# Kernel optimization log

Hardware: AMD Instinct MI355X
Metric: run time of the kernel (lower is better)

The kernel has to match this reference:

```python
import jax, jax.numpy as jnp
import numpy as np

B, T, D_IN, H, OUT = 512, 512, 64, 256, 64
EPS = 1e-5


def _ln(x, w, b):
    m = x.mean(-1, keepdims=True)
    v = ((x - m) ** 2).mean(-1, keepdims=True)
    return (x - m) / jnp.sqrt(v + EPS) * w + b


def _cell(x, h_prev, Wg, bg, gnw, gnb, Wc, bc, cnw, cnb):
    # LayerNormGRU cell
    combined = jnp.concatenate([x, h_prev], axis=-1)          # [B, D+H]
    rz = _ln(combined @ Wg.T + bg, gnw, gnb)                  # [B, 2H]
    r, z = jnp.split(rz, 2, axis=-1)
    r, z = jax.nn.sigmoid(r), jax.nn.sigmoid(z)
    combined_r = jnp.concatenate([x, r * h_prev], axis=-1)
    n = jnp.tanh(_ln(combined_r @ Wc.T + bc, cnw, cnb))       # [B, H]
    return (1.0 - z) * h_prev + z * n


def setup_inputs() -> dict:
    key = jax.random.key(0)
    ks = jax.random.split(key, 24)

    def uni(k, shape, fan_in):
        lim = 1.0 / np.sqrt(fan_in)
        return jax.random.uniform(k, shape, jnp.float32, -lim, lim)

    d0 = D_IN + H   # layer 0 cell input width
    d1 = H + H      # layer 1 cell input width
    return {
        "x": jax.random.normal(ks[0], (B, T, D_IN), jnp.float32),
        # layer 0
        "Wg0": uni(ks[1], (2 * H, d0), d0), "bg0": uni(ks[2], (2 * H,), d0),
        "gnw0": jnp.ones((2 * H,), jnp.float32), "gnb0": jnp.zeros((2 * H,), jnp.float32),
        "Wc0": uni(ks[3], (H, d0), d0), "bc0": uni(ks[4], (H,), d0),
        "cnw0": jnp.ones((H,), jnp.float32), "cnb0": jnp.zeros((H,), jnp.float32),
        # layer 1
        "Wg1": uni(ks[5], (2 * H, d1), d1), "bg1": uni(ks[6], (2 * H,), d1),
        "gnw1": jnp.ones((2 * H,), jnp.float32), "gnb1": jnp.zeros((2 * H,), jnp.float32),
        "Wc1": uni(ks[7], (H, d1), d1), "bc1": uni(ks[8], (H,), d1),
        "cnw1": jnp.ones((H,), jnp.float32), "cnb1": jnp.zeros((H,), jnp.float32),
        # output head
        "fcW": uni(ks[9], (OUT, H), H), "fcb": uni(ks[10], (OUT,), H),
    }


def reference(x, Wg0, bg0, gnw0, gnb0, Wc0, bc0, cnw0, cnb0,
              Wg1, bg1, gnw1, gnb1, Wc1, bc1, cnw1, cnb1, fcW, fcb):
    b = x.shape[0]
    h_init = (jnp.zeros((b, H), x.dtype), jnp.zeros((b, H), x.dtype))

    def step(carry, xt):
        h0, h1 = carry
        h0 = _cell(xt, h0, Wg0, bg0, gnw0, gnb0, Wc0, bc0, cnw0, cnb0)
        h1 = _cell(h0, h1, Wg1, bg1, gnw1, gnb1, Wc1, bc1, cnw1, cnb1)
        return (h0, h1), None

    (h0, h1), _ = jax.lax.scan(step, h_init, jnp.swapaxes(x, 0, 1))  # scan over T
    return h1 @ fcW.T + fcb  # [B, OUT]
```

## Files before the change

kernel.cpp:

```cpp
#include <hip/hip_runtime.h>


#define B_   512
#define T_   512
#define DIN  64
#define H_   256
#define OUT_ 64
#define EPS_ 1e-5f

typedef __attribute__((ext_vector_type(8))) short bf16x8;
typedef __attribute__((ext_vector_type(4))) float f32x4;

__device__ __forceinline__ unsigned short f2bf(float f) {
  unsigned int u = __float_as_uint(f);
  u += 0x7fffu + ((u >> 16) & 1u);
  return (unsigned short)(u >> 16);
}
__device__ __forceinline__ float bfh(unsigned short u) {
  return __uint_as_float(((unsigned int)u) << 16);
}
__device__ __forceinline__ float sigm_(float x) {
  return __builtin_amdgcn_rcpf(1.f + __expf(-x));
}
__device__ __forceinline__ float tanh_(float x) {
  return 1.f - 2.f * __builtin_amdgcn_rcpf(__expf(2.f * x) + 1.f);
}
template<int C>
__device__ __forceinline__ float dpp_add(float v) {
  int r = __builtin_amdgcn_update_dpp(0, __float_as_int(v), C, 0xF, 0xF, false);
  return v + __int_as_float(r);
}
__device__ __forceinline__ float red16(float v) {
  v = dpp_add<0x121>(v);
  v = dpp_add<0x122>(v);
  v = dpp_add<0x124>(v);
  v = dpp_add<0x128>(v);
  return v;
}

#define PIN8A(a) asm volatile("" : "+a"(a[0]), "+a"(a[1]), "+a"(a[2]), "+a"(a[3]), \
                                   "+a"(a[4]), "+a"(a[5]), "+a"(a[6]), "+a"(a[7]))

__global__ void prep_frag(const float* __restrict__ w, unsigned short* __restrict__ dst,
                          int N, int Ksrc, int koff) {
  int gid = blockIdx.x * 256 + threadIdx.x;
  if (gid >= N * 256) return;
  int n = gid >> 8, k = gid & 255;
  int idx = (((n >> 4) * 8 + (k >> 5)) * 64 + ((n & 15) + 16 * ((k >> 3) & 3))) * 8 + (k & 7);
  dst[idx] = f2bf(w[(size_t)n * Ksrc + koff + k]);
}

__global__ void prep_wx(const float* __restrict__ wg, const float* __restrict__ wc,
                        unsigned short* __restrict__ dst, int KX, int Kg, int Kc) {
  int gid = blockIdx.x * 256 + threadIdx.x;
  if (gid >= 768 * KX) return;
  int n = gid / KX, k = gid - n * KX;
  float v = (n < 512) ? wg[(size_t)n * Kg + k] : wc[(size_t)(n - 512) * Kc + k];
  dst[gid] = f2bf(v);
}

__global__ void bias_cat(const float* __restrict__ bg, const float* __restrict__ bc,
                         float* __restrict__ dst) {
  int i = blockIdx.x * 256 + threadIdx.x;
  if (i < 768) dst[i] = (i < 512) ? bg[i] : bc[i - 512];
}

__device__ __forceinline__ void precomp_tile(
    const void* __restrict__ Asrc, const unsigned short* __restrict__ wx,
    const float* __restrict__ bias, unsigned short* __restrict__ Pc,
    int TC, int t0, int KX, int AFP32,
    int mi, int nb, unsigned short* A_s, unsigned short* B_s, int t256)
{
  const int lane = t256 & 63, wv = t256 >> 6;
  const int m0 = mi * 128;
  const int bt = m0 / (TC * 16);
  const int tt0 = (m0 - bt * TC * 16) >> 4;
  const int mq = wv >> 1, nq = wv & 1;
  const int crow0 = (lane >> 4) * 4;

  f32x4 acc[4][4];
#pragma unroll
  for (int i = 0; i < 4; ++i)
#pragma unroll
    for (int j = 0; j < 4; ++j) acc[i][j] = (f32x4){0, 0, 0, 0};

  for (int kb = 0; kb < (KX >> 6); ++kb) {
    __syncthreads();
#pragma unroll
    for (int it = 0; it < 4; ++it) {
      int s = t256 + it * 256;
      int rg = s >> 3, k8 = s & 7;
      int mt = rg >> 4, r15 = rg & 15;
      int dl = r15 + 16 * (k8 & 3), kc = k8 >> 2;
      if (AFP32) {
        const float* xp = (const float*)Asrc +
            (((size_t)(bt * 16 + r15)) * T_ + (t0 + tt0 + mt)) * DIN + kb * 64 + k8 * 8;
        float4 u0 = *(const float4*)xp, u1 = *(const float4*)(xp + 4);
        unsigned short tmp[8];
        tmp[0] = f2bf(u0.x); tmp[1] = f2bf(u0.y); tmp[2] = f2bf(u0.z); tmp[3] = f2bf(u0.w);
        tmp[4] = f2bf(u1.x); tmp[5] = f2bf(u1.y); tmp[6] = f2bf(u1.z); tmp[7] = f2bf(u1.w);
        *reinterpret_cast<bf16x8*>(&A_s[((mt * 2 + kc) * 64 + dl) * 8]) =
            *reinterpret_cast<bf16x8*>(tmp);
      } else {
        const unsigned short* ap = (const unsigned short*)Asrc +
            ((size_t)(m0 + rg)) * KX + kb * 64 + k8 * 8;
        *reinterpret_cast<bf16x8*>(&A_s[((mt * 2 + kc) * 64 + dl) * 8]) =
            *reinterpret_cast<const bf16x8*>(ap);
      }
      const unsigned short* bp = wx + ((size_t)(nb + rg)) * KX + kb * 64 + k8 * 8;
      *reinterpret_cast<bf16x8*>(&B_s[((mt * 2 + kc) * 64 + dl) * 8]) =
          *reinterpret_cast<const bf16x8*>(bp);
    }
    __syncthreads();
#pragma unroll
    for (int kc = 0; kc < 2; ++kc) {
      bf16x8 av[4], bv[4];
#pragma unroll
      for (int i = 0; i < 4; ++i) {
        av[i] = *reinterpret_cast<const bf16x8*>(&A_s[(((mq * 4 + i) * 2 + kc) * 64 + lane) * 8]);
        bv[i] = *reinterpret_cast<const bf16x8*>(&B_s[(((nq * 4 + i) * 2 + kc) * 64 + lane) * 8]);
      }
#pragma unroll
      for (int i = 0; i < 4; ++i)
#pragma unroll
        for (int j = 0; j < 4; ++j)
          acc[i][j] = __builtin_amdgcn_mfma_f32_16x16x32_bf16(av[i], bv[j], acc[i][j], 0, 0, 0);
    }
  }
  float bb[4];
#pragma unroll
  for (int j = 0; j < 4; ++j) bb[j] = bias[nb + nq * 64 + j * 16 + (lane & 15)];
#pragma unroll
  for (int i = 0; i < 4; ++i) {
    int tt = tt0 + mq * 4 + i;
#pragma unroll
    for (int j = 0; j < 4; ++j) {
      int n = nb + nq * 64 + j * 16 + (lane & 15);
      ushort4 o;
      o.x = f2bf(acc[i][j][0] + bb[j]); o.y = f2bf(acc[i][j][1] + bb[j]);
      o.z = f2bf(acc[i][j][2] + bb[j]); o.w = f2bf(acc[i][j][3] + bb[j]);
      *reinterpret_cast<ushort4*>(&Pc[((size_t)(bt * TC + tt) * 768 + n) * 16 + crow0]) = o;
    }
  }
}

__launch_bounds__(256)
__global__ void precomp_std(const void* __restrict__ Asrc,
                            const unsigned short* __restrict__ wx,
                            const float* __restrict__ bias,
                            unsigned short* __restrict__ Pc,
                            int TC, int t0, int KX, int AFP32) {
  __shared__ __align__(16) unsigned short A_s[8192];
  __shared__ __align__(16) unsigned short B_s[8192];
  precomp_tile(Asrc, wx, bias, Pc, TC, t0, KX, AFP32,
               blockIdx.x, blockIdx.y * 128, A_s, B_s, threadIdx.x);
}

__device__ __forceinline__ void gru_body(
    unsigned char* smem, int bt,
    const unsigned short* __restrict__ gfrag,
    const unsigned short* __restrict__ cfrag,
    const unsigned short* __restrict__ Pc,
    const float* __restrict__ gnw, const float* __restrict__ gnb,
    const float* __restrict__ cnw, const float* __restrict__ cnb,
    float* __restrict__ hstate, unsigned short* __restrict__ h0out,
    int TC, int first)
{
  unsigned short* wc_s = (unsigned short*)smem;
  unsigned short (*h_s)[264]  = (unsigned short(*)[264])(smem + 131072);
  unsigned short (*rh_s)[264] = (unsigned short(*)[264])(smem + 139520);
  float (*sumP)[20] = (float(*)[20])(smem + 147968);
  float (*sqP)[20]  = (float(*)[20])(smem + 148608);

  const int tid = threadIdx.x, lane = tid & 63, wv = tid >> 6;
  const int b0 = bt * 16;
  const int arow = lane & 15, koff = (lane >> 4) * 8, crow0 = (lane >> 4) * 4;
  const int colr0 = 32 * wv + (lane & 15), colr1 = colr0 + 16;
  const int nt0 = 2 * wv, nt1 = 2 * wv + 1, nt2 = 16 + 2 * wv, nt3 = 17 + 2 * wv;

  for (int i = tid; i < 8192; i += 512)
    *reinterpret_cast<bf16x8*>(&wc_s[i * 8]) = *reinterpret_cast<const bf16x8*>(&cfrag[i * 8]);

  bf16x8 wgr0[8], wgr1[8], wgr2[8], wgr3[8];
#pragma unroll
  for (int kc = 0; kc < 8; ++kc) {
    wgr0[kc] = *reinterpret_cast<const bf16x8*>(&gfrag[((nt0 * 8 + kc) * 64 + lane) * 8]);
    wgr1[kc] = *reinterpret_cast<const bf16x8*>(&gfrag[((nt1 * 8 + kc) * 64 + lane) * 8]);
    wgr2[kc] = *reinterpret_cast<const bf16x8*>(&gfrag[((nt2 * 8 + kc) * 64 + lane) * 8]);
    wgr3[kc] = *reinterpret_cast<const bf16x8*>(&gfrag[((nt3 * 8 + kc) * 64 + lane) * 8]);
  }

  const float gw_r0 = gnw[colr0], gb_r0 = gnb[colr0];
  const float gw_r1 = gnw[colr1], gb_r1 = gnb[colr1];
  const float gw_z0 = gnw[256 + colr0], gb_z0 = gnb[256 + colr0];
  const float gw_z1 = gnw[256 + colr1], gb_z1 = gnb[256 + colr1];
  const float cw0 = cnw[colr0], cb0 = cnb[colr0];
  const float cw1 = cnw[colr1], cb1 = cnb[colr1];

  float hm[2][4];
  if (first) {
#pragma unroll
    for (int g = 0; g < 4; ++g) { hm[0][g] = 0.f; hm[1][g] = 0.f; }
    for (int i = tid; i < 16 * 264; i += 512) (&h_s[0][0])[i] = 0;
  } else {
#pragma unroll
    for (int g = 0; g < 4; ++g) {
      hm[0][g] = hstate[(size_t)(b0 + crow0 + g) * 256 + colr0];
      hm[1][g] = hstate[(size_t)(b0 + crow0 + g) * 256 + colr1];
    }
    int r = tid >> 5, c8 = (tid & 31) * 8;
    float4 v0 = *reinterpret_cast<const float4*>(&hstate[(size_t)(b0 + r) * 256 + c8]);
    float4 v1 = *reinterpret_cast<const float4*>(&hstate[(size_t)(b0 + r) * 256 + c8 + 4]);
    ushort4 o0, o1;
    o0.x = f2bf(v0.x); o0.y = f2bf(v0.y); o0.z = f2bf(v0.z); o0.w = f2bf(v0.w);
    o1.x = f2bf(v1.x); o1.y = f2bf(v1.y); o1.z = f2bf(v1.z); o1.w = f2bf(v1.w);
    *reinterpret_cast<ushort4*>(&h_s[r][c8]) = o0;
    *reinterpret_cast<ushort4*>(&h_s[r][c8 + 4]) = o1;
  }
  __syncthreads();

  const unsigned short* Pr = Pc + ((size_t)bt * TC * 768 + colr0) * 16;
  ushort4 npr0 = *reinterpret_cast<const ushort4*>(Pr + crow0);
  ushort4 npr1 = *reinterpret_cast<const ushort4*>(Pr + 256 + crow0);
  ushort4 npz0 = *reinterpret_cast<const ushort4*>(Pr + 4096 + crow0);
  ushort4 npz1 = *reinterpret_cast<const ushort4*>(Pr + 4352 + crow0);
  ushort4 npn0 = *reinterpret_cast<const ushort4*>(Pr + 8192 + crow0);
  ushort4 npn1 = *reinterpret_cast<const ushort4*>(Pr + 8448 + crow0);

  for (int tt = 0; tt < TC; ++tt) {
    PIN8A(wgr0); PIN8A(wgr1); PIN8A(wgr2); PIN8A(wgr3);

    ushort4 pr0 = npr0, pr1 = npr1, pz0 = npz0, pz1 = npz1, pn0 = npn0, pn1 = npn1;
    if (tt + 1 < TC) {
      Pr += 12288;
      npr0 = *reinterpret_cast<const ushort4*>(Pr + crow0);
      npr1 = *reinterpret_cast<const ushort4*>(Pr + 256 + crow0);
      npz0 = *reinterpret_cast<const ushort4*>(Pr + 4096 + crow0);
      npz1 = *reinterpret_cast<const ushort4*>(Pr + 4352 + crow0);
      npn0 = *reinterpret_cast<const ushort4*>(Pr + 8192 + crow0);
      npn1 = *reinterpret_cast<const ushort4*>(Pr + 8448 + crow0);
    }

    f32x4 a0 = {0, 0, 0, 0}, a1 = {0, 0, 0, 0}, a2 = {0, 0, 0, 0}, a3 = {0, 0, 0, 0};
#pragma unroll
    for (int kc = 0; kc < 8; ++kc) {
      bf16x8 av = *reinterpret_cast<const bf16x8*>(&h_s[arow][kc * 32 + koff]);
      a0 = __builtin_amdgcn_mfma_f32_16x16x32_bf16(av, wgr0[kc], a0, 0, 0, 0);
      a1 = __builtin_amdgcn_mfma_f32_16x16x32_bf16(av, wgr1[kc], a1, 0, 0, 0);
      a2 = __builtin_amdgcn_mfma_f32_16x16x32_bf16(av, wgr2[kc], a2, 0, 0, 0);
      a3 = __builtin_amdgcn_mfma_f32_16x16x32_bf16(av, wgr3[kc], a3, 0, 0, 0);
    }
    float vr0[4], vr1[4], vz0[4], vz1[4];
    {
      float s4[4], q4[4];
#pragma unroll
      for (int g = 0; g < 4; ++g) {
        vr0[g] = a0[g] + bfh(((const unsigned short*)&pr0)[g]);
        vr1[g] = a1[g] + bfh(((const unsigned short*)&pr1)[g]);
        vz0[g] = a2[g] + bfh(((const unsigned short*)&pz0)[g]);
        vz1[g] = a3[g] + bfh(((const unsigned short*)&pz1)[g]);
        s4[g] = red16(vr0[g] + vr1[g] + vz0[g] + vz1[g]);
        q4[g] = red16(vr0[g] * vr0[g] + vr1[g] * vr1[g] + vz0[g] * vz0[g] + vz1[g] * vz1[g]);
      }
      if ((lane & 15) == 0) {
        *reinterpret_cast<f32x4*>(&sumP[wv][crow0]) = (f32x4){s4[0], s4[1], s4[2], s4[3]};
        *reinterpret_cast<f32x4*>(&sqP[wv][crow0])  = (f32x4){q4[0], q4[1], q4[2], q4[3]};
      }
    }
    __syncthreads();

    float zf[2][4];
    {
      int sg = lane >> 4, rr = lane & 15;
      float S = sumP[2 * sg][rr] + sumP[2 * sg + 1][rr];
      float Q = sqP[2 * sg][rr] + sqP[2 * sg + 1][rr];
      S += __shfl_xor(S, 16, 64); Q += __shfl_xor(Q, 16, 64);
      S += __shfl_xor(S, 32, 64); Q += __shfl_xor(Q, 32, 64);
      float mn = S * (1.f / 512.f);
      float rs = __builtin_amdgcn_rsqf(Q * (1.f / 512.f) - mn * mn + EPS_);
#pragma unroll
      for (int g = 0; g < 4; ++g) {
        float m_ = __shfl(mn, crow0 + g, 64);
        float r_ = __shfl(rs, crow0 + g, 64);
        float rv0 = sigm_(fmaf((vr0[g] - m_) * r_, gw_r0, gb_r0));
        float rv1 = sigm_(fmaf((vr1[g] - m_) * r_, gw_r1, gb_r1));
        zf[0][g]  = sigm_(fmaf((vz0[g] - m_) * r_, gw_z0, gb_z0));
        zf[1][g]  = sigm_(fmaf((vz1[g] - m_) * r_, gw_z1, gb_z1));
        rh_s[crow0 + g][colr0] = f2bf(rv0 * hm[0][g]);
        rh_s[crow0 + g][colr1] = f2bf(rv1 * hm[1][g]);
      }
    }
    __syncthreads();

    f32x4 c0a = {0, 0, 0, 0}, c1a = {0, 0, 0, 0};
#pragma unroll
    for (int kc = 0; kc < 8; ++kc) {
      bf16x8 av = *reinterpret_cast<const bf16x8*>(&rh_s[arow][kc * 32 + koff]);
      bf16x8 b0v = *reinterpret_cast<const bf16x8*>(&wc_s[((nt0 * 8 + kc) * 64 + lane) * 8]);
      bf16x8 b1v = *reinterpret_cast<const bf16x8*>(&wc_s[((nt1 * 8 + kc) * 64 + lane) * 8]);
      c0a = __builtin_amdgcn_mfma_f32_16x16x32_bf16(av, b0v, c0a, 0, 0, 0);
      c1a = __builtin_amdgcn_mfma_f32_16x16x32_bf16(av, b1v, c1a, 0, 0, 0);
    }
    float vc0[4], vc1[4];
    {
      float s4[4], q4[4];
#pragma unroll
      for (int g = 0; g < 4; ++g) {
        vc0[g] = c0a[g] + bfh(((const unsigned short*)&pn0)[g]);
        vc1[g] = c1a[g] + bfh(((const unsigned short*)&pn1)[g]);
        s4[g] = red16(vc0[g] + vc1[g]);
        q4[g] = red16(vc0[g] * vc0[g] + vc1[g] * vc1[g]);
      }
      if ((lane & 15) == 0) {
        *reinterpret_cast<f32x4*>(&sumP[wv][crow0]) = (f32x4){s4[0], s4[1], s4[2], s4[3]};
        *reinterpret_cast<f32x4*>(&sqP[wv][crow0])  = (f32x4){q4[0], q4[1], q4[2], q4[3]};
      }
    }
    __syncthreads();

    {
      int sg = lane >> 4, rr = lane & 15;
      float S = sumP[2 * sg][rr] + sumP[2 * sg + 1][rr];
      float Q = sqP[2 * sg][rr] + sqP[2 * sg + 1][rr];
      S += __shfl_xor(S, 16, 64); Q += __shfl_xor(Q, 16, 64);
      S += __shfl_xor(S, 32, 64); Q += __shfl_xor(Q, 32, 64);
      float mn = S * (1.f / 256.f);
      float rs = __builtin_amdgcn_rsqf(Q * (1.f / 256.f) - mn * mn + EPS_);
      unsigned short* hrow = h0out ? (h0out + (size_t)(bt * TC + tt) * 4096) : (unsigned short*)nullptr;
#pragma unroll
      for (int g = 0; g < 4; ++g) {
        float m_ = __shfl(mn, crow0 + g, 64);
        float r_ = __shfl(rs, crow0 + g, 64);
        float n0 = tanh_(fmaf((vc0[g] - m_) * r_, cw0, cb0));
        float n1 = tanh_(fmaf((vc1[g] - m_) * r_, cw1, cb1));
        float h0n = fmaf(zf[0][g], n0 - hm[0][g], hm[0][g]);
        float h1n = fmaf(zf[1][g], n1 - hm[1][g], hm[1][g]);
        hm[0][g] = h0n; hm[1][g] = h1n;
        unsigned short hb0 = f2bf(h0n), hb1 = f2bf(h1n);
        h_s[crow0 + g][colr0] = hb0;
        h_s[crow0 + g][colr1] = hb1;
        if (hrow) {
          hrow[(size_t)(crow0 + g) * 256 + colr0] = hb0;
          hrow[(size_t)(crow0 + g) * 256 + colr1] = hb1;
        }
      }
    }
    __syncthreads();
  }

#pragma unroll
  for (int g = 0; g < 4; ++g) {
    hstate[(size_t)(b0 + crow0 + g) * 256 + colr0] = hm[0][g];
    hstate[(size_t)(b0 + crow0 + g) * 256 + colr1] = hm[1][g];
  }
}

__launch_bounds__(512, 2)
__global__ void mega(
    const float* __restrict__ x,
    const unsigned short* __restrict__ g0h, const unsigned short* __restrict__ c0h,
    const unsigned short* __restrict__ g1h, const unsigned short* __restrict__ c1h,
    const unsigned short* __restrict__ wx0, const unsigned short* __restrict__ wx1,
    const float* __restrict__ b768_0, const float* __restrict__ b768_1,
    const float* __restrict__ gnw0, const float* __restrict__ gnb0,
    const float* __restrict__ cnw0, const float* __restrict__ cnb0,
    const float* __restrict__ gnw1, const float* __restrict__ gnb1,
    const float* __restrict__ cnw1, const float* __restrict__ cnb1,
    float* __restrict__ hst0, float* __restrict__ hst1,
    unsigned short* __restrict__ P0a, unsigned short* __restrict__ P0b,
    unsigned short* __restrict__ P1a, unsigned short* __restrict__ P1b,
    unsigned short* __restrict__ h0a, unsigned short* __restrict__ h0b,
    int k, int TC, int NC)
{
  __shared__ __align__(16) unsigned char smem[149504];
  const int bid = blockIdx.x;

  if (bid < 32) {
    if (k >= NC) return;
    unsigned short* P0 = (k & 1) ? P0b : P0a;
    unsigned short* h0 = (k & 1) ? h0b : h0a;
    gru_body(smem, bid, g0h, c0h, P0, gnw0, gnb0, cnw0, cnb0, hst0, h0, TC, k == 0);
  } else if (bid < 64) {
    int kD = k - 2;
    if (kD < 0 || kD >= NC) return;
    unsigned short* P1 = (kD & 1) ? P1b : P1a;
    gru_body(smem, bid - 32, g1h, c1h, P1, gnw1, gnb1, cnw1, cnb1, hst1,
             (unsigned short*)nullptr, TC, kD == 0);
  } else if (bid < 160) {
    int kA = k + 1;
    if (kA >= NC) return;
    unsigned short* P0 = (kA & 1) ? P0b : P0a;
    int team = (bid - 64) * 2 + (threadIdx.x >> 8);
    int t256 = threadIdx.x & 255;
    unsigned short* A_s = (unsigned short*)(smem + (threadIdx.x >> 8) * 32768);
    unsigned short* B_s = A_s + 8192;
    int ntile = 24 * TC;
    for (int i = team; i < ntile; i += 192) {
      int mi = i % (4 * TC), ni = i / (4 * TC);
      precomp_tile(x, wx0, b768_0, P0, TC, kA * TC, 64, 1, mi, ni * 128, A_s, B_s, t256);
    }
  } else {
    int kC = k - 1;
    if (kC < 0 || kC >= NC) return;
    const unsigned short* h0 = (kC & 1) ? h0b : h0a;
    unsigned short* P1 = (kC & 1) ? P1b : P1a;
    int team = (bid - 160) * 2 + (threadIdx.x >> 8);
    int t256 = threadIdx.x & 255;
    unsigned short* A_s = (unsigned short*)(smem + (threadIdx.x >> 8) * 32768);
    unsigned short* B_s = A_s + 8192;
    int ntile = 24 * TC;
    for (int i = team; i < ntile; i += 192) {
      int mi = i % (4 * TC), ni = i / (4 * TC);
      precomp_tile(h0, wx1, b768_1, P1, TC, 0, 256, 0, mi, ni * 128, A_s, B_s, t256);
    }
  }
}

__launch_bounds__(256)
__global__ void head_k(const float* __restrict__ h1, const float* __restrict__ fcW,
                       const float* __restrict__ fcb, float* __restrict__ out) {
  __shared__ float hs[16][256];
  const int tid = threadIdx.x, b0 = blockIdx.x * 16;
  for (int i = tid; i < 16 * 64; i += 256) {
    int r = i >> 6, c4 = (i & 63) * 4;
    *reinterpret_cast<float4*>(&hs[r][c4]) =
        *reinterpret_cast<const float4*>(&h1[(size_t)(b0 + r) * 256 + c4]);
  }
  __syncthreads();
  int r = tid >> 4, o = (tid & 15) * 4;
  float a0 = fcb[o], a1 = fcb[o + 1], a2 = fcb[o + 2], a3 = fcb[o + 3];
  for (int k = 0; k < 256; ++k) {
    float h = hs[r][k];
    a0 = fmaf(h, fcW[(size_t)(o + 0) * 256 + k], a0);
    a1 = fmaf(h, fcW[(size_t)(o + 1) * 256 + k], a1);
    a2 = fmaf(h, fcW[(size_t)(o + 2) * 256 + k], a2);
    a3 = fmaf(h, fcW[(size_t)(o + 3) * 256 + k], a3);
  }
  float4 ov = {a0, a1, a2, a3};
  *reinterpret_cast<float4*>(&out[(size_t)(b0 + r) * 64 + o]) = ov;
}

extern "C" void kernel_launch(void* const* d_in, const int* in_sizes, int n_in,
                              void* d_out, int out_size, void* d_ws, size_t ws_size,
                              hipStream_t stream) {
  (void)in_sizes; (void)n_in; (void)out_size;
  const float* x    = (const float*)d_in[0];
  const float* Wg0  = (const float*)d_in[1];
  const float* bg0  = (const float*)d_in[2];
  const float* gnw0 = (const float*)d_in[3];
  const float* gnb0 = (const float*)d_in[4];
  const float* Wc0  = (const float*)d_in[5];
  const float* bc0  = (const float*)d_in[6];
  const float* cnw0 = (const float*)d_in[7];
  const float* cnb0 = (const float*)d_in[8];
  const float* Wg1  = (const float*)d_in[9];
  const float* bg1  = (const float*)d_in[10];
  const float* gnw1 = (const float*)d_in[11];
  const float* gnb1 = (const float*)d_in[12];
  const float* Wc1  = (const float*)d_in[13];
  const float* bc1  = (const float*)d_in[14];
  const float* cnw1 = (const float*)d_in[15];
  const float* cnb1 = (const float*)d_in[16];
  const float* fcW  = (const float*)d_in[17];
  const float* fcb  = (const float*)d_in[18];

  float* hst0 = (float*)d_ws;
  float* hst1 = hst0 + 131072;
  float* b768_0 = hst1 + 131072;
  float* b768_1 = b768_0 + 768;
  unsigned short* g0h = (unsigned short*)(b768_1 + 768);
  unsigned short* c0h = g0h + 131072;
  unsigned short* g1h = c0h + 65536;
  unsigned short* c1h = g1h + 131072;
  unsigned short* wx0 = c1h + 65536;
  unsigned short* wx1 = wx0 + 49152;
  unsigned short* dynbase = wx1 + 196608;

  const size_t fixed_bytes = (size_t)((char*)dynbase - (char*)d_ws);
  int TC = 32;
  while (TC > 4) {
    size_t need = fixed_bytes + (size_t)TC * 3670016;
    if (need <= ws_size) break;
    TC >>= 1;
  }
  const int NC = T_ / TC;

  unsigned short* P0a = dynbase;
  unsigned short* P0b = P0a + (size_t)TC * 393216;
  unsigned short* P1a = P0b + (size_t)TC * 393216;
  unsigned short* P1b = P1a + (size_t)TC * 393216;
  unsigned short* h0a = P1b + (size_t)TC * 393216;
  unsigned short* h0b = h0a + (size_t)TC * 131072;

  prep_frag<<<512, 256, 0, stream>>>(Wg0, g0h, 512, 320, 64);
  prep_frag<<<256, 256, 0, stream>>>(Wc0, c0h, 256, 320, 64);
  prep_frag<<<512, 256, 0, stream>>>(Wg1, g1h, 512, 512, 256);
  prep_frag<<<256, 256, 0, stream>>>(Wc1, c1h, 256, 512, 256);
  prep_wx<<<192, 256, 0, stream>>>(Wg0, Wc0, wx0, 64, 320, 320);
  prep_wx<<<768, 256, 0, stream>>>(Wg1, Wc1, wx1, 256, 512, 512);
  bias_cat<<<3, 256, 0, stream>>>(bg0, bc0, b768_0);
  bias_cat<<<3, 256, 0, stream>>>(bg1, bc1, b768_1);

  precomp_std<<<dim3(4 * TC, 6), 256, 0, stream>>>(x, wx0, b768_0, P0a, TC, 0, 64, 1);

  for (int k = 0; k < NC + 2; ++k) {
    mega<<<256, 512, 0, stream>>>(x, g0h, c0h, g1h, c1h, wx0, wx1, b768_0, b768_1,
        gnw0, gnb0, cnw0, cnb0, gnw1, gnb1, cnw1, cnb1,
        hst0, hst1, P0a, P0b, P1a, P1b, h0a, h0b, k, TC, NC);
  }

  head_k<<<32, 256, 0, stream>>>(hst1, fcW, fcb, (float*)d_out);
}
```

Before: 2.630 ms.

## Hold all GRU weights in registers with 4-wave blocks, drop LDS weight staging

The recurrent GRU body moves from 8 waves to 4 waves per block, with each wave owning 64 columns. All three weight sets (r, z gates and candidate) now live in registers, two in AGPRs and one in VGPRs, so the candidate weights are no longer staged through 128KB of LDS each step. LayerNorm params are staged in LDS, and the row mean/rstd is broadcast through LDS instead of shuffles. The precompute partitions are re-split for the smaller blocks. This removes per-step LDS weight reads and one level of cross-wave reduction, at the cost of very high register pressure, possible spills, less parallelism per recurrence block, and dropping the P-tile prefetch into loads issued within the same step.

```diff
diff --git a/kernel.cpp b/kernel.cpp
--- a/kernel.cpp
+++ b/kernel.cpp
@@ -40,6 +40,8 @@
 
 #define PIN8A(a) asm volatile("" : "+a"(a[0]), "+a"(a[1]), "+a"(a[2]), "+a"(a[3]), \
                                    "+a"(a[4]), "+a"(a[5]), "+a"(a[6]), "+a"(a[7]))
+#define PIN8V(a) asm volatile("" : "+v"(a[0]), "+v"(a[1]), "+v"(a[2]), "+v"(a[3]), \
+                                   "+v"(a[4]), "+v"(a[5]), "+v"(a[6]), "+v"(a[7]))
 
 __global__ void prep_frag(const float* __restrict__ w, unsigned short* __restrict__ dst,
                           int N, int Ksrc, int koff) {
@@ -166,101 +168,100 @@
     float* __restrict__ hstate, unsigned short* __restrict__ h0out,
     int TC, int first)
 {
-  unsigned short* wc_s = (unsigned short*)smem;
-  unsigned short (*h_s)[264]  = (unsigned short(*)[264])(smem + 131072);
-  unsigned short (*rh_s)[264] = (unsigned short(*)[264])(smem + 139520);
-  float (*sumP)[20] = (float(*)[20])(smem + 147968);
-  float (*sqP)[20]  = (float(*)[20])(smem + 148608);
+  unsigned short (*h_s)[264]  = (unsigned short(*)[264])(smem);
+  unsigned short (*rh_s)[264] = (unsigned short(*)[264])(smem + 8448);
+  float (*sumP)[20] = (float(*)[20])(smem + 16896);
+  float (*sqP)[20]  = (float(*)[20])(smem + 17216);
+  float2* mnrs = (float2*)(smem + 17536);
+  float2* pg   = (float2*)(smem + 17664);
+  float2* pc   = (float2*)(smem + 21760);
 
   const int tid = threadIdx.x, lane = tid & 63, wv = tid >> 6;
   const int b0 = bt * 16;
   const int arow = lane & 15, koff = (lane >> 4) * 8, crow0 = (lane >> 4) * 4;
-  const int colr0 = 32 * wv + (lane & 15), colr1 = colr0 + 16;
-  const int nt0 = 2 * wv, nt1 = 2 * wv + 1, nt2 = 16 + 2 * wv, nt3 = 17 + 2 * wv;
-
-  for (int i = tid; i < 8192; i += 512)
-    *reinterpret_cast<bf16x8*>(&wc_s[i * 8]) = *reinterpret_cast<const bf16x8*>(&cfrag[i * 8]);
-
-  bf16x8 wgr0[8], wgr1[8], wgr2[8], wgr3[8];
-#pragma unroll
-  for (int kc = 0; kc < 8; ++kc) {
-    wgr0[kc] = *reinterpret_cast<const bf16x8*>(&gfrag[((nt0 * 8 + kc) * 64 + lane) * 8]);
-    wgr1[kc] = *reinterpret_cast<const bf16x8*>(&gfrag[((nt1 * 8 + kc) * 64 + lane) * 8]);
-    wgr2[kc] = *reinterpret_cast<const bf16x8*>(&gfrag[((nt2 * 8 + kc) * 64 + lane) * 8]);
-    wgr3[kc] = *reinterpret_cast<const bf16x8*>(&gfrag[((nt3 * 8 + kc) * 64 + lane) * 8]);
-  }
-
-  const float gw_r0 = gnw[colr0], gb_r0 = gnb[colr0];
-  const float gw_r1 = gnw[colr1], gb_r1 = gnb[colr1];
-  const float gw_z0 = gnw[256 + colr0], gb_z0 = gnb[256 + colr0];
-  const float gw_z1 = gnw[256 + colr1], gb_z1 = gnb[256 + colr1];
-  const float cw0 = cnw[colr0], cb0 = cnb[colr0];
-  const float cw1 = cnw[colr1], cb1 = cnb[colr1];
-
-  float hm[2][4];
+
+  pg[tid] = make_float2(gnw[tid], gnb[tid]);
+  pg[256 + tid] = make_float2(gnw[256 + tid], gnb[256 + tid]);
+  pc[tid] = make_float2(cnw[tid], cnb[tid]);
+
+  bf16x8 wgr[4][8], wgz[4][8], wcd[4][8];
+#pragma unroll
+  for (int j = 0; j < 4; ++j) {
+    const int rn = 4 * wv + j, zn = 16 + 4 * wv + j;
+#pragma unroll
+    for (int kc = 0; kc < 8; ++kc) {
+      wgr[j][kc] = *reinterpret_cast<const bf16x8*>(&gfrag[((rn * 8 + kc) * 64 + lane) * 8]);
+      wgz[j][kc] = *reinterpret_cast<const bf16x8*>(&gfrag[((zn * 8 + kc) * 64 + lane) * 8]);
+      wcd[j][kc] = *reinterpret_cast<const bf16x8*>(&cfrag[((rn * 8 + kc) * 64 + lane) * 8]);
+    }
+  }
+
+  float hm[4][4];
   if (first) {
 #pragma unroll
-    for (int g = 0; g < 4; ++g) { hm[0][g] = 0.f; hm[1][g] = 0.f; }
-    for (int i = tid; i < 16 * 264; i += 512) (&h_s[0][0])[i] = 0;
+    for (int j = 0; j < 4; ++j)
+#pragma unroll
+      for (int g = 0; g < 4; ++g) hm[j][g] = 0.f;
+    for (int i = tid; i < 16 * 264; i += 256) (&h_s[0][0])[i] = 0;
   } else {
 #pragma unroll
-    for (int g = 0; g < 4; ++g) {
-      hm[0][g] = hstate[(size_t)(b0 + crow0 + g) * 256 + colr0];
-      hm[1][g] = hstate[(size_t)(b0 + crow0 + g) * 256 + colr1];
-    }
-    int r = tid >> 5, c8 = (tid & 31) * 8;
-    float4 v0 = *reinterpret_cast<const float4*>(&hstate[(size_t)(b0 + r) * 256 + c8]);
-    float4 v1 = *reinterpret_cast<const float4*>(&hstate[(size_t)(b0 + r) * 256 + c8 + 4]);
-    ushort4 o0, o1;
-    o0.x = f2bf(v0.x); o0.y = f2bf(v0.y); o0.z = f2bf(v0.z); o0.w = f2bf(v0.w);
-    o1.x = f2bf(v1.x); o1.y = f2bf(v1.y); o1.z = f2bf(v1.z); o1.w = f2bf(v1.w);
-    *reinterpret_cast<ushort4*>(&h_s[r][c8]) = o0;
-    *reinterpret_cast<ushort4*>(&h_s[r][c8 + 4]) = o1;
+    for (int j = 0; j < 4; ++j) {
+      const int cj = 64 * wv + 16 * j + (lane & 15);
+#pragma unroll
+      for (int g = 0; g < 4; ++g)
+        hm[j][g] = hstate[(size_t)(b0 + crow0 + g) * 256 + cj];
+    }
+    int r = tid >> 4, c16 = (tid & 15) * 16;
+#pragma unroll
+    for (int q = 0; q < 4; ++q) {
+      float4 v = *reinterpret_cast<const float4*>(&hstate[(size_t)(b0 + r) * 256 + c16 + 4 * q]);
+      ushort4 o;
+      o.x = f2bf(v.x); o.y = f2bf(v.y); o.z = f2bf(v.z); o.w = f2bf(v.w);
+      *reinterpret_cast<ushort4*>(&h_s[r][c16 + 4 * q]) = o;
+    }
   }
   __syncthreads();
 
-  const unsigned short* Pr = Pc + ((size_t)bt * TC * 768 + colr0) * 16;
-  ushort4 npr0 = *reinterpret_cast<const ushort4*>(Pr + crow0);
-  ushort4 npr1 = *reinterpret_cast<const ushort4*>(Pr + 256 + crow0);
-  ushort4 npz0 = *reinterpret_cast<const ushort4*>(Pr + 4096 + crow0);
-  ushort4 npz1 = *reinterpret_cast<const ushort4*>(Pr + 4352 + crow0);
-  ushort4 npn0 = *reinterpret_cast<const ushort4*>(Pr + 8192 + crow0);
-  ushort4 npn1 = *reinterpret_cast<const ushort4*>(Pr + 8448 + crow0);
+  const unsigned short* Pb = Pc + (size_t)bt * TC * 768 * 16;
 
   for (int tt = 0; tt < TC; ++tt) {
-    PIN8A(wgr0); PIN8A(wgr1); PIN8A(wgr2); PIN8A(wgr3);
-
-    ushort4 pr0 = npr0, pr1 = npr1, pz0 = npz0, pz1 = npz1, pn0 = npn0, pn1 = npn1;
-    if (tt + 1 < TC) {
-      Pr += 12288;
-      npr0 = *reinterpret_cast<const ushort4*>(Pr + crow0);
-      npr1 = *reinterpret_cast<const ushort4*>(Pr + 256 + crow0);
-      npz0 = *reinterpret_cast<const ushort4*>(Pr + 4096 + crow0);
-      npz1 = *reinterpret_cast<const ushort4*>(Pr + 4352 + crow0);
-      npn0 = *reinterpret_cast<const ushort4*>(Pr + 8192 + crow0);
-      npn1 = *reinterpret_cast<const ushort4*>(Pr + 8448 + crow0);
-    }
-
-    f32x4 a0 = {0, 0, 0, 0}, a1 = {0, 0, 0, 0}, a2 = {0, 0, 0, 0}, a3 = {0, 0, 0, 0};
+    PIN8A(wgr[0]); PIN8A(wgr[1]); PIN8A(wgr[2]); PIN8A(wgr[3]);
+    PIN8A(wgz[0]); PIN8A(wgz[1]); PIN8A(wgz[2]); PIN8A(wgz[3]);
+    PIN8V(wcd[0]); PIN8V(wcd[1]); PIN8V(wcd[2]); PIN8V(wcd[3]);
+
+    ushort4 pr4[4], pz4[4];
+#pragma unroll
+    for (int j = 0; j < 4; ++j) {
+      const int cj = 64 * wv + 16 * j + (lane & 15);
+      pr4[j] = *reinterpret_cast<const ushort4*>(Pb + (size_t)cj * 16 + crow0);
+      pz4[j] = *reinterpret_cast<const ushort4*>(Pb + (size_t)(256 + cj) * 16 + crow0);
+    }
+
+    f32x4 ar[4] = {{0,0,0,0},{0,0,0,0},{0,0,0,0},{0,0,0,0}};
+    f32x4 az[4] = {{0,0,0,0},{0,0,0,0},{0,0,0,0},{0,0,0,0}};
 #pragma unroll
     for (int kc = 0; kc < 8; ++kc) {
       bf16x8 av = *reinterpret_cast<const bf16x8*>(&h_s[arow][kc * 32 + koff]);
-      a0 = __builtin_amdgcn_mfma_f32_16x16x32_bf16(av, wgr0[kc], a0, 0, 0, 0);
-      a1 = __builtin_amdgcn_mfma_f32_16x16x32_bf16(av, wgr1[kc], a1, 0, 0, 0);
-      a2 = __builtin_amdgcn_mfma_f32_16x16x32_bf16(av, wgr2[kc], a2, 0, 0, 0);
-      a3 = __builtin_amdgcn_mfma_f32_16x16x32_bf16(av, wgr3[kc], a3, 0, 0, 0);
-    }
-    float vr0[4], vr1[4], vz0[4], vz1[4];
+#pragma unroll
+      for (int j = 0; j < 4; ++j) {
+        ar[j] = __builtin_amdgcn_mfma_f32_16x16x32_bf16(av, wgr[j][kc], ar[j], 0, 0, 0);
+        az[j] = __builtin_amdgcn_mfma_f32_16x16x32_bf16(av, wgz[j][kc], az[j], 0, 0, 0);
+      }
+    }
+    float vr[4][4], vz[4][4];
     {
       float s4[4], q4[4];
 #pragma unroll
       for (int g = 0; g < 4; ++g) {
-        vr0[g] = a0[g] + bfh(((const unsigned short*)&pr0)[g]);
-        vr1[g] = a1[g] + bfh(((const unsigned short*)&pr1)[g]);
-        vz0[g] = a2[g] + bfh(((const unsigned short*)&pz0)[g]);
-        vz1[g] = a3[g] + bfh(((const unsigned short*)&pz1)[g]);
-        s4[g] = red16(vr0[g] + vr1[g] + vz0[g] + vz1[g]);
-        q4[g] = red16(vr0[g] * vr0[g] + vr1[g] * vr1[g] + vz0[g] * vz0[g] + vz1[g] * vz1[g]);
+        float s = 0.f, q = 0.f;
+#pragma unroll
+        for (int j = 0; j < 4; ++j) {
+          vr[j][g] = ar[j][g] + bfh(((const unsigned short*)&pr4[j])[g]);
+          vz[j][g] = az[j][g] + bfh(((const unsigned short*)&pz4[j])[g]);
+          s += vr[j][g] + vz[j][g];
+          q += vr[j][g] * vr[j][g] + vz[j][g] * vz[j][g];
+        }
+        s4[g] = red16(s); q4[g] = red16(q);
       }
       if ((lane & 15) == 0) {
         *reinterpret_cast<f32x4*>(&sumP[wv][crow0]) = (f32x4){s4[0], s4[1], s4[2], s4[3]};
@@ -269,47 +270,57 @@
     }
     __syncthreads();
 
-    float zf[2][4];
+    float zf[4][4];
     {
-      int sg = lane >> 4, rr = lane & 15;
-      float S = sumP[2 * sg][rr] + sumP[2 * sg + 1][rr];
-      float Q = sqP[2 * sg][rr] + sqP[2 * sg + 1][rr];
-      S += __shfl_xor(S, 16, 64); Q += __shfl_xor(Q, 16, 64);
-      S += __shfl_xor(S, 32, 64); Q += __shfl_xor(Q, 32, 64);
+      int rr = lane & 15;
+      float S = sumP[0][rr] + sumP[1][rr] + sumP[2][rr] + sumP[3][rr];
+      float Q = sqP[0][rr] + sqP[1][rr] + sqP[2][rr] + sqP[3][rr];
       float mn = S * (1.f / 512.f);
       float rs = __builtin_amdgcn_rsqf(Q * (1.f / 512.f) - mn * mn + EPS_);
+      if (lane < 16) mnrs[lane] = make_float2(mn, rs);
+    }
+#pragma unroll
+    for (int j = 0; j < 4; ++j) {
+      const int cj = 64 * wv + 16 * j + (lane & 15);
+      float2 prm_r = pg[cj], prm_z = pg[256 + cj];
 #pragma unroll
       for (int g = 0; g < 4; ++g) {
-        float m_ = __shfl(mn, crow0 + g, 64);
-        float r_ = __shfl(rs, crow0 + g, 64);
-        float rv0 = sigm_(fmaf((vr0[g] - m_) * r_, gw_r0, gb_r0));
-        float rv1 = sigm_(fmaf((vr1[g] - m_) * r_, gw_r1, gb_r1));
-        zf[0][g]  = sigm_(fmaf((vz0[g] - m_) * r_, gw_z0, gb_z0));
-        zf[1][g]  = sigm_(fmaf((vz1[g] - m_) * r_, gw_z1, gb_z1));
-        rh_s[crow0 + g][colr0] = f2bf(rv0 * hm[0][g]);
-        rh_s[crow0 + g][colr1] = f2bf(rv1 * hm[1][g]);
+        float2 mr = mnrs[crow0 + g];
+        float rv = sigm_(fmaf((vr[j][g] - mr.x) * mr.y, prm_r.x, prm_r.y));
+        zf[j][g] = sigm_(fmaf((vz[j][g] - mr.x) * mr.y, prm_z.x, prm_z.y));
+        rh_s[crow0 + g][cj] = f2bf(rv * hm[j][g]);
       }
     }
     __syncthreads();
 
-    f32x4 c0a = {0, 0, 0, 0}, c1a = {0, 0, 0, 0};
+    ushort4 pn4[4];
+#pragma unroll
+    for (int j = 0; j < 4; ++j) {
+      const int cj = 64 * wv + 16 * j + (lane & 15);
+      pn4[j] = *reinterpret_cast<const ushort4*>(Pb + (size_t)(512 + cj) * 16 + crow0);
+    }
+
+    f32x4 ac[4] = {{0,0,0,0},{0,0,0,0},{0,0,0,0},{0,0,0,0}};
 #pragma unroll
     for (int kc = 0; kc < 8; ++kc) {
       bf16x8 av = *reinterpret_cast<const bf16x8*>(&rh_s[arow][kc * 32 + koff]);
-      bf16x8 b0v = *reinterpret_cast<const bf16x8*>(&wc_s[((nt0 * 8 + kc) * 64 + lane) * 8]);
-      bf16x8 b1v = *reinterpret_cast<const bf16x8*>(&wc_s[((nt1 * 8 + kc) * 64 + lane) * 8]);
-      c0a = __builtin_amdgcn_mfma_f32_16x16x32_bf16(av, b0v, c0a, 0, 0, 0);
-      c1a = __builtin_amdgcn_mfma_f32_16x16x32_bf16(av, b1v, c1a, 0, 0, 0);
-    }
-    float vc0[4], vc1[4];
+#pragma unroll
+      for (int j = 0; j < 4; ++j)
+        ac[j] = __builtin_amdgcn_mfma_f32_16x16x32_bf16(av, wcd[j][kc], ac[j], 0, 0, 0);
+    }
+    float vc[4][4];
     {
       float s4[4], q4[4];
 #pragma unroll
       for (int g = 0; g < 4; ++g) {
-        vc0[g] = c0a[g] + bfh(((const unsigned short*)&pn0)[g]);
-        vc1[g] = c1a[g] + bfh(((const unsigned short*)&pn1)[g]);
-        s4[g] = red16(vc0[g] + vc1[g]);
-        q4[g] = red16(vc0[g] * vc0[g] + vc1[g] * vc1[g]);
+        float s = 0.f, q = 0.f;
+#pragma unroll
+        for (int j = 0; j < 4; ++j) {
+          vc[j][g] = ac[j][g] + bfh(((const unsigned short*)&pn4[j])[g]);
+          s += vc[j][g];
+          q += vc[j][g] * vc[j][g];
+        }
+        s4[g] = red16(s); q4[g] = red16(q);
       }
       if ((lane & 15) == 0) {
         *reinterpret_cast<f32x4*>(&sumP[wv][crow0]) = (f32x4){s4[0], s4[1], s4[2], s4[3]};
@@ -319,43 +330,43 @@
     __syncthreads();
 
     {
-      int sg = lane >> 4, rr = lane & 15;
-      float S = sumP[2 * sg][rr] + sumP[2 * sg + 1][rr];
-      float Q = sqP[2 * sg][rr] + sqP[2 * sg + 1][rr];
-      S += __shfl_xor(S, 16, 64); Q += __shfl_xor(Q, 16, 64);
-      S += __shfl_xor(S, 32, 64); Q += __shfl_xor(Q, 32, 64);
+      int rr = lane & 15;
+      float S = sumP[0][rr] + sumP[1][rr] + sumP[2][rr] + sumP[3][rr];
+      float Q = sqP[0][rr] + sqP[1][rr] + sqP[2][rr] + sqP[3][rr];
       float mn = S * (1.f / 256.f);
       float rs = __builtin_amdgcn_rsqf(Q * (1.f / 256.f) - mn * mn + EPS_);
-      unsigned short* hrow = h0out ? (h0out + (size_t)(bt * TC + tt) * 4096) : (unsigned short*)nullptr;
+      if (lane < 16) mnrs[lane] = make_float2(mn, rs);
+    }
+    unsigned short* hrow = h0out ? (h0out + (size_t)(bt * TC + tt) * 4096) : (unsigned short*)nullptr;
+#pragma unroll
+    for (int j = 0; j < 4; ++j) {
+      const int cj = 64 * wv + 16 * j + (lane & 15);
+      float2 prm_c = pc[cj];
 #pragma unroll
       for (int g = 0; g < 4; ++g) {
-        float m_ = __shfl(mn, crow0 + g, 64);
-        float r_ = __shfl(rs, crow0 + g, 64);
-        float n0 = tanh_(fmaf((vc0[g] - m_) * r_, cw0, cb0));
-        float n1 = tanh_(fmaf((vc1[g] - m_) * r_, cw1, cb1));
-        float h0n = fmaf(zf[0][g], n0 - hm[0][g], hm[0][g]);
-        float h1n = fmaf(zf[1][g], n1 - hm[1][g], hm[1][g]);
-        hm[0][g] = h0n; hm[1][g] = h1n;
-        unsigned short hb0 = f2bf(h0n), hb1 = f2bf(h1n);
-        h_s[crow0 + g][colr0] = hb0;
-        h_s[crow0 + g][colr1] = hb1;
-        if (hrow) {
-          hrow[(size_t)(crow0 + g) * 256 + colr0] = hb0;
-          hrow[(size_t)(crow0 + g) * 256 + colr1] = hb1;
-        }
+        float2 mr = mnrs[crow0 + g];
+        float nv = tanh_(fmaf((vc[j][g] - mr.x) * mr.y, prm_c.x, prm_c.y));
+        float h = fmaf(zf[j][g], nv - hm[j][g], hm[j][g]);
+        hm[j][g] = h;
+        unsigned short hb = f2bf(h);
+        h_s[crow0 + g][cj] = hb;
+        if (hrow) hrow[(size_t)(crow0 + g) * 256 + cj] = hb;
       }
     }
     __syncthreads();
-  }
-
-#pragma unroll
-  for (int g = 0; g < 4; ++g) {
-    hstate[(size_t)(b0 + crow0 + g) * 256 + colr0] = hm[0][g];
-    hstate[(size_t)(b0 + crow0 + g) * 256 + colr1] = hm[1][g];
-  }
-}
-
-__launch_bounds__(512, 2)
+    Pb += 12288;
+  }
+
+#pragma unroll
+  for (int j = 0; j < 4; ++j) {
+    const int cj = 64 * wv + 16 * j + (lane & 15);
+#pragma unroll
+    for (int g = 0; g < 4; ++g)
+      hstate[(size_t)(b0 + crow0 + g) * 256 + cj] = hm[j][g];
+  }
+}
+
+__launch_bounds__(256, 1)
 __global__ void mega(
     const float* __restrict__ x,
     const unsigned short* __restrict__ g0h, const unsigned short* __restrict__ c0h,
@@ -372,7 +383,7 @@
     unsigned short* __restrict__ h0a, unsigned short* __restrict__ h0b,
     int k, int TC, int NC)
 {
-  __shared__ __align__(16) unsigned char smem[149504];
+  __shared__ __align__(16) unsigned char smem[32768];
   const int bid = blockIdx.x;
 
   if (bid < 32) {
@@ -386,32 +397,28 @@
     unsigned short* P1 = (kD & 1) ? P1b : P1a;
     gru_body(smem, bid - 32, g1h, c1h, P1, gnw1, gnb1, cnw1, cnb1, hst1,
              (unsigned short*)nullptr, TC, kD == 0);
-  } else if (bid < 160) {
+  } else if (bid < 128) {
     int kA = k + 1;
     if (kA >= NC) return;
     unsigned short* P0 = (kA & 1) ? P0b : P0a;
-    int team = (bid - 64) * 2 + (threadIdx.x >> 8);
-    int t256 = threadIdx.x & 255;
-    unsigned short* A_s = (unsigned short*)(smem + (threadIdx.x >> 8) * 32768);
+    unsigned short* A_s = (unsigned short*)smem;
     unsigned short* B_s = A_s + 8192;
     int ntile = 24 * TC;
-    for (int i = team; i < ntile; i += 192) {
+    for (int i = bid - 64; i < ntile; i += 64) {
       int mi = i % (4 * TC), ni = i / (4 * TC);
-      precomp_tile(x, wx0, b768_0, P0, TC, kA * TC, 64, 1, mi, ni * 128, A_s, B_s, t256);
+      precomp_tile(x, wx0, b768_0, P0, TC, kA * TC, 64, 1, mi, ni * 128, A_s, B_s, threadIdx.x);
     }
   } else {
     int kC = k - 1;
     if (kC < 0 || kC >= NC) return;
     const unsigned short* h0 = (kC & 1) ? h0b : h0a;
     unsigned short* P1 = (kC & 1) ? P1b : P1a;
-    int team = (bid - 160) * 2 + (threadIdx.x >> 8);
-    int t256 = threadIdx.x & 255;
-    unsigned short* A_s = (unsigned short*)(smem + (threadIdx.x >> 8) * 32768);
+    unsigned short* A_s = (unsigned short*)smem;
     unsigned short* B_s = A_s + 8192;
     int ntile = 24 * TC;
-    for (int i = team; i < ntile; i += 192) {
+    for (int i = bid - 128; i < ntile; i += 128) {
       int mi = i % (4 * TC), ni = i / (4 * TC);
-      precomp_tile(h0, wx1, b768_1, P1, TC, 0, 256, 0, mi, ni * 128, A_s, B_s, t256);
+      precomp_tile(h0, wx1, b768_1, P1, TC, 0, 256, 0, mi, ni * 128, A_s, B_s, threadIdx.x);
     }
   }
 }
@@ -504,7 +511,7 @@
   precomp_std<<<dim3(4 * TC, 6), 256, 0, stream>>>(x, wx0, b768_0, P0a, TC, 0, 64, 1);
 
   for (int k = 0; k < NC + 2; ++k) {
-    mega<<<256, 512, 0, stream>>>(x, g0h, c0h, g1h, c1h, wx0, wx1, b768_0, b768_1,
+    mega<<<256, 256, 0, stream>>>(x, g0h, c0h, g1h, c1h, wx0, wx1, b768_0, b768_1,
         gnw0, gnb0, cnw0, cnb0, gnw1, gnb1, cnw1, cnb1,
         hst0, hst1, P0a, P0b, P1a, P1b, h0a, h0b, k, TC, NC);
   }
```

New measurement: 5.249 ms. +99.6%, slower.
